# Optimization experiments

Measured on AMD Instinct MI355X. Metric: run time of the kernel, lower is better.

Reference implementation:

```python
import jax, jax.numpy as jnp
import numpy as np
import math

D_MODEL = 256
D_STATE = 16
D_CONV = 4
EXPAND = 2
N_HEADS = 4
D_INNER = EXPAND * D_MODEL          # 512
DT_RANK = (D_MODEL + 15) // 16      # 16
B_SZ, SEQ = 4, 2048


def setup_inputs() -> dict:
    key = jax.random.key(0)
    ks = jax.random.split(key, 12)
    rn = lambda i, shp, sc=0.02: jax.random.normal(ks[i], shp, dtype=jnp.float32) * sc
    x = jax.random.normal(ks[0], (B_SZ, SEQ, D_MODEL), dtype=jnp.float32)
    return dict(
        x=x,
        ln_g=jnp.ones((D_MODEL,), jnp.float32),
        ln_b=jnp.zeros((D_MODEL,), jnp.float32),
        W_in=rn(1, (D_MODEL, 2 * D_INNER)),
        conv_w=rn(2, (D_INNER, D_CONV), 0.1),
        conv_b=jnp.zeros((D_INNER,), jnp.float32),
        W_xproj=rn(3, (D_INNER, DT_RANK + 2 * D_STATE)),
        W_dt=rn(4, (DT_RANK, D_INNER), 0.1),
        b_dt=jnp.full((D_INNER,), -4.6, jnp.float32),  # softplus ~ 0.01 init
        A_log=jnp.log(jnp.tile(jnp.arange(1, D_STATE + 1, dtype=jnp.float32), (D_INNER, 1))),
        Dp=jnp.ones((D_INNER,), jnp.float32),
        W_out_m=rn(5, (D_INNER, D_MODEL)),
        W_qkv=rn(6, (D_MODEL, 3 * D_MODEL)),
        b_qkv=jnp.zeros((3 * D_MODEL,), jnp.float32),
        W_o=rn(7, (D_MODEL, D_MODEL)),
        b_o=jnp.zeros((D_MODEL,), jnp.float32),
        W_gate=rn(8, (2 * D_MODEL, D_MODEL)),
        b_gate=jnp.zeros((D_MODEL,), jnp.float32),
    )


def _sssd_forward(x, ln_g, ln_b, W_in, conv_w, conv_b, W_xproj, W_dt, b_dt,
                  A_log, Dp, W_out_m, W_qkv, b_qkv, W_o, b_o, W_gate, b_gate):
    B, L, D = x.shape
    # LayerNorm
    mu = x.mean(-1, keepdims=True)
    var = x.var(-1, keepdims=True)
    xn = (x - mu) * jax.lax.rsqrt(var + 1e-5) * ln_g + ln_b

    # ---- Mamba branch ----
    xz = xn @ W_in                      # (B,L,2*D_INNER)
    xm, z = jnp.split(xz, 2, axis=-1)
    # causal depthwise conv1d (kernel D_CONV)
    xp = jnp.pad(xm, ((0, 0), (D_CONV - 1, 0), (0, 0)))
    xc = conv_b + sum(xp[:, k:k + L, :] * conv_w[:, k] for k in range(D_CONV))
    xc = jax.nn.silu(xc)
    dbl = xc @ W_xproj                  # (B,L,DT_RANK+2*D_STATE)
    dt_in = dbl[..., :DT_RANK]
    Bm = dbl[..., DT_RANK:DT_RANK + D_STATE]
    Cm = dbl[..., DT_RANK + D_STATE:]
    dt = jax.nn.softplus(dt_in @ W_dt + b_dt)   # (B,L,D_INNER)
    A = -jnp.exp(A_log)                 # (D_INNER, D_STATE)

    def step(h, inp):
        x_t, dt_t, B_t, C_t = inp       # (B,Din),(B,Din),(B,N),(B,N)
        dA = jnp.exp(dt_t[..., None] * A)               # (B,Din,N)
        h = dA * h + (dt_t * x_t)[..., None] * B_t[:, None, :]
        y = jnp.einsum('bdn,bn->bd', h, C_t)
        return h, y

    h0 = jnp.zeros((B, D_INNER, D_STATE), x.dtype)
    xs = (jnp.swapaxes(xc, 0, 1), jnp.swapaxes(dt, 0, 1),
          jnp.swapaxes(Bm, 0, 1), jnp.swapaxes(Cm, 0, 1))
    _, ys = jax.lax.scan(step, h0, xs)
    y = jnp.swapaxes(ys, 0, 1) + xc * Dp
    y = y * jax.nn.silu(z)
    ssm_out = y @ W_out_m               # (B,L,D)

    # ---- MHSA branch (eval: no dropout) ----
    hd = D // N_HEADS
    qkv = xn @ W_qkv + b_qkv
    q, k, v = jnp.split(qkv, 3, axis=-1)
    sh = lambda t: t.reshape(B, L, N_HEADS, hd).transpose(0, 2, 1, 3)
    q, k, v = sh(q), sh(k), sh(v)
    scores = jnp.einsum('bhqd,bhkd->bhqk', q, k) * (1.0 / math.sqrt(hd))
    attn = jax.nn.softmax(scores, axis=-1)
    o = jnp.einsum('bhqk,bhkd->bhqd', attn, v).transpose(0, 2, 1, 3).reshape(B, L, D)
    attn_out = o @ W_o + b_o

    # ---- sigmoid gate fusion ----
    gate = jax.nn.sigmoid(jnp.concatenate([ssm_out, attn_out], axis=-1) @ W_gate + b_gate)
    fused = gate * ssm_out + (1.0 - gate) * attn_out
    return x + fused


def reference(x, ln_g, ln_b, W_in, conv_w, conv_b, W_xproj, W_dt, b_dt,
              A_log, Dp, W_out_m, W_qkv, b_qkv, W_o, b_o, W_gate, b_gate):
    return _sssd_forward(x, ln_g, ln_b, W_in, conv_w, conv_b, W_xproj, W_dt, b_dt,
                         A_log, Dp, W_out_m, W_qkv, b_qkv, W_o, b_o, W_gate, b_gate)
```

## Files before the change

kernel.cpp:

```cpp
#include <hip/hip_runtime.h>
#include <math.h>

#define B_SZ 4
#define SEQ 2048
#define DM 256
#define DI 512
#define DS 16
#define DTR 16
#define NH 4
#define HD 64
#define T_TOK (B_SZ*SEQ)
#define NCH 64
#define CL (SEQ/NCH)

typedef short bf16x8 __attribute__((ext_vector_type(8)));
typedef float f32x4  __attribute__((ext_vector_type(4)));
typedef unsigned short u16;

__device__ __forceinline__ float sigmoidf_(float x){ return 1.f/(1.f+__expf(-x)); }
__device__ __forceinline__ u16 f2bf(float x){
  unsigned int u = __float_as_uint(x);
  u += 0x7fffu + ((u>>16)&1u);
  return (u16)(u>>16);
}

__global__ __launch_bounds__(64) void tcvt_kernel(const float* __restrict__ src,
    u16* __restrict__ dst, int N, int K) {
  int n = blockIdx.x*64 + threadIdx.x;
  int k = blockIdx.y;
  dst[(size_t)n*K + k] = f2bf(src[(size_t)k*N + n]);
}

__global__ __launch_bounds__(64) void tcvt_pad_kernel(const float* __restrict__ src,
    u16* __restrict__ dst, int K, int Nvalid) {
  int n = threadIdx.x;
  int k = blockIdx.y;
  dst[(size_t)n*K + k] = (n < Nvalid) ? f2bf(src[(size_t)k*Nvalid + n]) : (u16)0;
}

__global__ __launch_bounds__(256) void ln_kernel(const float* __restrict__ x,
    const float* __restrict__ g, const float* __restrict__ b,
    u16* __restrict__ xn_bf) {
  int wid = threadIdx.x >> 6;
  int lane = threadIdx.x & 63;
  int token = blockIdx.x*4 + wid;
  const float* xr = x + (size_t)token*DM;
  float4 v = *(const float4*)&xr[lane*4];
  float s  = v.x+v.y+v.z+v.w;
  float ss = v.x*v.x+v.y*v.y+v.z*v.z+v.w*v.w;
  for (int m=1;m<64;m<<=1){ s += __shfl_xor(s,m); ss += __shfl_xor(ss,m); }
  float mu  = s * (1.f/DM);
  float var = ss*(1.f/DM) - mu*mu;
  float rs  = rsqrtf(var + 1e-5f);
  float4 gv = *(const float4*)&g[lane*4];
  float4 bv = *(const float4*)&b[lane*4];
  ushort4 o;
  o.x = f2bf((v.x-mu)*rs*gv.x + bv.x);
  o.y = f2bf((v.y-mu)*rs*gv.y + bv.y);
  o.z = f2bf((v.z-mu)*rs*gv.z + bv.z);
  o.w = f2bf((v.w-mu)*rs*gv.w + bv.w);
  *(ushort4*)&xn_bf[(size_t)token*DM + lane*4] = o;
}

template<int ACT>
__global__ __launch_bounds__(256) void gemm_mfma(const u16* __restrict__ A,
    const u16* __restrict__ Wt, const float* __restrict__ bias,
    float* __restrict__ C, u16* __restrict__ Cbf, int K, int ldc, int nvalid) {
  __shared__ u16 lds[12288];
  int tid = threadIdx.x;
  int m0 = blockIdx.y*128, n0 = blockIdx.x*64;
  int w = tid>>6, l = tid&63, lq = l&15, lg = l>>4;
  int wm = w>>1, wn = w&1;
  f32x4 acc[4][2] = {};
  for (int k0 = 0; k0 < K; k0 += 64) {
#pragma unroll
    for (int i=0;i<4;++i){
      int gid = i*256 + tid;
      int row = gid>>3, g = gid&7;
      *(bf16x8*)&lds[row*64 + ((g ^ (row&7))*8)] =
          *(const bf16x8*)&A[(size_t)(m0+row)*K + k0 + g*8];
    }
#pragma unroll
    for (int i=0;i<2;++i){
      int gid = i*256 + tid;
      int row = gid>>3, g = gid&7;
      *(bf16x8*)&lds[8192 + row*64 + ((g ^ (row&7))*8)] =
          *(const bf16x8*)&Wt[(size_t)(n0+row)*K + k0 + g*8];
    }
    __syncthreads();
#pragma unroll
    for (int ks=0;ks<2;++ks){
      bf16x8 af[4], bfv[2];
#pragma unroll
      for (int mi=0;mi<4;++mi){
        int row = wm*64 + mi*16 + lq;
        af[mi] = *(bf16x8*)&lds[row*64 + (((ks*4+lg) ^ (row&7))*8)];
      }
#pragma unroll
      for (int nj=0;nj<2;++nj){
        int row = wn*32 + nj*16 + lq;
        bfv[nj] = *(bf16x8*)&lds[8192 + row*64 + (((ks*4+lg) ^ (row&7))*8)];
      }
#pragma unroll
      for (int mi=0;mi<4;++mi)
#pragma unroll
        for (int nj=0;nj<2;++nj)
          acc[mi][nj] = __builtin_amdgcn_mfma_f32_16x16x32_bf16(af[mi], bfv[nj], acc[mi][nj], 0,0,0);
    }
    __syncthreads();
  }
#pragma unroll
  for (int mi=0;mi<4;++mi){
#pragma unroll
    for (int nj=0;nj<2;++nj){
#pragma unroll
      for (int r=0;r<4;++r){
        int row = m0 + wm*64 + mi*16 + lg*4 + r;
        int col = n0 + wn*32 + nj*16 + lq;
        if (col < nvalid) {
          float v = acc[mi][nj][r];
          if (bias) v += bias[col];
          if (ACT==1) v = sigmoidf_(v);
          if (C)   C[(size_t)row*ldc + col] = v;
          if (Cbf) Cbf[(size_t)row*ldc + col] = f2bf(v);
        }
      }
    }
  }
}

__global__ __launch_bounds__(256) void conv_kernel(const float* __restrict__ xz,
    const float* __restrict__ cw, const float* __restrict__ cb,
    float* __restrict__ xc, u16* __restrict__ xc_bf) {
  int idx = blockIdx.x*256 + threadIdx.x;
  int d = idx & (DI-1);
  int t = idx >> 9;
  int l = t & (SEQ-1);
  float acc = cb[d];
  float w0=cw[d*4+0], w1=cw[d*4+1], w2=cw[d*4+2], w3=cw[d*4+3];
  const float* base = xz + (size_t)t*1024 + d;
  if (l>=3) acc += base[-3*1024]*w0;
  if (l>=2) acc += base[-2*1024]*w1;
  if (l>=1) acc += base[-1*1024]*w2;
  acc += base[0]*w3;
  float v = acc * sigmoidf_(acc);
  xc[idx] = v;
  xc_bf[idx] = f2bf(v);
}

__global__ __launch_bounds__(256) void dt_kernel(const float* __restrict__ dbl,
    const float* __restrict__ Wdt, const float* __restrict__ bdt,
    float* __restrict__ dt) {
  __shared__ float sdbl[4][16];
  int wid = threadIdx.x>>6, lane = threadIdx.x&63;
  int token = blockIdx.x*4 + wid;
  if (lane < 16) sdbl[wid][lane] = dbl[(size_t)token*48 + lane];
  __syncthreads();
  float din[16];
#pragma unroll
  for (int k=0;k<16;++k) din[k] = sdbl[wid][k];
#pragma unroll
  for (int r=0;r<8;++r){
    int d = lane + r*64;
    float acc = bdt[d];
#pragma unroll
    for (int k=0;k<16;++k) acc += din[k]*Wdt[k*DI+d];
    float sp = (acc > 20.f) ? acc : log1pf(__expf(acc));
    dt[(size_t)token*DI+d] = sp;
  }
}

__global__ __launch_bounds__(512) void scan_p1(const float* __restrict__ xc,
    const float* __restrict__ dt, const float* __restrict__ dbl,
    const float* __restrict__ A_log, float* __restrict__ Pws, float* __restrict__ Hws) {
  __shared__ float sB[CL][16];
  int d = threadIdx.x;
  int bc = blockIdx.x;
  int b = bc >> 6, c = bc & 63;
  {
    int t = threadIdx.x >> 4, n = threadIdx.x & 15;
    sB[t][n] = dbl[((size_t)b*SEQ + c*CL + t)*48 + DTR + n];
  }
  __syncthreads();
  float An[16];
#pragma unroll
  for (int i=0;i<4;++i){
    float4 a = *(const float4*)&A_log[d*16 + i*4];
    An[i*4+0] = -__expf(a.x); An[i*4+1] = -__expf(a.y);
    An[i*4+2] = -__expf(a.z); An[i*4+3] = -__expf(a.w);
  }
  float h[16] = {};
  float P[16];
#pragma unroll
  for (int n=0;n<16;++n) P[n] = 1.f;
  size_t tok = (size_t)b*SEQ + c*CL;
  for (int t=0;t<CL;++t,++tok){
    float dtv = dt[tok*DI+d];
    float xcv = xc[tok*DI+d];
    float u = dtv*xcv;
    float4 B0 = *(float4*)&sB[t][0];
    float4 B1 = *(float4*)&sB[t][4];
    float4 B2 = *(float4*)&sB[t][8];
    float4 B3 = *(float4*)&sB[t][12];
    float Bv[16] = {B0.x,B0.y,B0.z,B0.w,B1.x,B1.y,B1.z,B1.w,
                    B2.x,B2.y,B2.z,B2.w,B3.x,B3.y,B3.z,B3.w};
#pragma unroll
    for (int n=0;n<16;++n){
      float e = __expf(dtv*An[n]);
      P[n] *= e;
      h[n] = e*h[n] + u*Bv[n];
    }
  }
  size_t base = (((size_t)b*NCH + c)*DI + d)*16;
#pragma unroll
  for (int n=0;n<16;++n){ Pws[base+n] = P[n]; Hws[base+n] = h[n]; }
}

__global__ __launch_bounds__(256) void scan_combine(const float* __restrict__ Pws,
    const float* __restrict__ Hws, float* __restrict__ H0ws) {
  int gid = blockIdx.x*256 + threadIdx.x;
  int b  = gid >> 13;
  int dn = gid & 8191;
  float h0 = 0.f;
#pragma unroll 4
  for (int c=0;c<NCH;++c){
    size_t idx = ((size_t)(b*NCH+c)<<13) + dn;
    H0ws[idx] = h0;
    h0 = Pws[idx]*h0 + Hws[idx];
  }
}

__global__ __launch_bounds__(512) void scan_p2(const float* __restrict__ xc,
    const float* __restrict__ dt, const float* __restrict__ dbl,
    const float* __restrict__ A_log, const float* __restrict__ Dp,
    const float* __restrict__ xz, const float* __restrict__ H0ws,
    u16* __restrict__ ygate_bf) {
  __shared__ float sBC[CL][32];
  int d = threadIdx.x;
  int bc = blockIdx.x;
  int b = bc >> 6, c = bc & 63;
#pragma unroll
  for (int i=0;i<2;++i){
    int idx = i*512 + threadIdx.x;
    int t = idx >> 5, q = idx & 31;
    sBC[t][q] = dbl[((size_t)b*SEQ + c*CL + t)*48 + DTR + q];
  }
  __syncthreads();
  float An[16];
#pragma unroll
  for (int i=0;i<4;++i){
    float4 a = *(const float4*)&A_log[d*16 + i*4];
    An[i*4+0] = -__expf(a.x); An[i*4+1] = -__expf(a.y);
    An[i*4+2] = -__expf(a.z); An[i*4+3] = -__expf(a.w);
  }
  float Dd = Dp[d];
  float h[16];
  size_t base = (((size_t)b*NCH + c)*DI + d)*16;
#pragma unroll
  for (int i=0;i<4;++i){
    float4 h4 = *(const float4*)&H0ws[base + i*4];
    h[i*4+0]=h4.x; h[i*4+1]=h4.y; h[i*4+2]=h4.z; h[i*4+3]=h4.w;
  }
  size_t tok = (size_t)b*SEQ + c*CL;
  for (int t=0;t<CL;++t,++tok){
    float dtv = dt[tok*DI+d];
    float xcv = xc[tok*DI+d];
    float zv  = xz[tok*1024 + DI + d];
    float u = dtv*xcv;
    float4 B0 = *(float4*)&sBC[t][0];
    float4 B1 = *(float4*)&sBC[t][4];
    float4 B2 = *(float4*)&sBC[t][8];
    float4 B3 = *(float4*)&sBC[t][12];
    float4 C0 = *(float4*)&sBC[t][16];
    float4 C1 = *(float4*)&sBC[t][20];
    float4 C2 = *(float4*)&sBC[t][24];
    float4 C3 = *(float4*)&sBC[t][28];
    float Bv[16] = {B0.x,B0.y,B0.z,B0.w,B1.x,B1.y,B1.z,B1.w,
                    B2.x,B2.y,B2.z,B2.w,B3.x,B3.y,B3.z,B3.w};
    float Cv[16] = {C0.x,C0.y,C0.z,C0.w,C1.x,C1.y,C1.z,C1.w,
                    C2.x,C2.y,C2.z,C2.w,C3.x,C3.y,C3.z,C3.w};
    float y = 0.f;
#pragma unroll
    for (int n=0;n<16;++n){
      float e = __expf(dtv*An[n]);
      h[n] = e*h[n] + u*Bv[n];
      y += h[n]*Cv[n];
    }
    y += xcv*Dd;
    ygate_bf[tok*DI + d] = f2bf(y * (zv*sigmoidf_(zv)));
  }
}

__global__ __launch_bounds__(256) void vt_kernel(const u16* __restrict__ qkvb,
    u16* __restrict__ vT) {
  int bh = blockIdx.y; int b = bh>>2, h = bh&3;
  int l0 = blockIdx.x*64;
  int d = threadIdx.x & 63;
  int oct = threadIdx.x >> 6;
  u16 tmp[16];
#pragma unroll
  for (int i=0;i<16;++i){
    int l = l0 + oct*16 + i;
    tmp[i] = qkvb[((size_t)b*SEQ + l)*768 + 512 + h*HD + d];
  }
  size_t dst = ((size_t)bh*HD + d)*SEQ + l0 + oct*16;
  *(bf16x8*)&vT[dst]   = *(bf16x8*)&tmp[0];
  *(bf16x8*)&vT[dst+8] = *(bf16x8*)&tmp[8];
}

__global__ __launch_bounds__(256) void attn_mfma_kernel(const u16* __restrict__ qkvb,
    const u16* __restrict__ vT,
    float* __restrict__ Opart, float* __restrict__ ml) {
  __shared__ u16 lds[12288];
  int bh = blockIdx.y; int b = bh>>2, h = bh&3;
  int s = blockIdx.z;
  int tid = threadIdx.x;
  int w = tid>>6, l = tid&63;
  int lq = l & 15;
  int lg = l >> 4;
  size_t bbase = (size_t)b*SEQ;
  size_t vbase = (size_t)bh*HD*SEQ;
  int q0 = blockIdx.x*64 + w*16;

  bf16x8 qf[2];
#pragma unroll
  for (int dsl=0; dsl<2; ++dsl)
    qf[dsl] = *(const bf16x8*)&qkvb[(bbase + q0 + lq)*768 + h*HD + lg*8 + dsl*32];

  float m_ = -1e30f, l_ = 0.f;
  f32x4 oacc[4] = {{0,0,0,0},{0,0,0,0},{0,0,0,0},{0,0,0,0}};
  int pbase = 8192 + w*1024;

  for (int kt=s*8; kt<s*8+8; ++kt){
    __syncthreads();
#pragma unroll
    for (int i=0;i<2;++i){
      int gid = i*256 + tid;
      int row = gid>>3, g = gid&7;
      *(bf16x8*)&lds[row*64 + ((g ^ (row&7))*8)] =
          *(const bf16x8*)&qkvb[(bbase + kt*64 + row)*768 + 256 + h*HD + g*8];
    }
#pragma unroll
    for (int i=0;i<2;++i){
      int gid = i*256 + tid;
      int row = gid>>3, g = gid&7;
      *(bf16x8*)&lds[4096 + row*64 + ((g ^ (row&7))*8)] =
          *(const bf16x8*)&vT[vbase + (size_t)row*SEQ + kt*64 + g*8];
    }
    __syncthreads();

    f32x4 sacc[4] = {{0,0,0,0},{0,0,0,0},{0,0,0,0},{0,0,0,0}};
    __builtin_amdgcn_s_setprio(1);
#pragma unroll
    for (int kg=0;kg<4;++kg){
#pragma unroll
      for (int dsl=0;dsl<2;++dsl){
        int row = kg*16 + lq;
        bf16x8 kf = *(bf16x8*)&lds[row*64 + (((dsl*4 + lg) ^ (row&7))*8)];
        sacc[kg] = __builtin_amdgcn_mfma_f32_16x16x32_bf16(kf, qf[dsl], sacc[kg], 0,0,0);
      }
    }
    __builtin_amdgcn_s_setprio(0);

    float tm = sacc[0][0];
#pragma unroll
    for (int kg=0;kg<4;++kg){
      float a = fmaxf(fmaxf(sacc[kg][0],sacc[kg][1]),fmaxf(sacc[kg][2],sacc[kg][3]));
      tm = fmaxf(tm, a);
    }
    tm *= 0.125f;
    tm = fmaxf(tm, __shfl_xor(tm,16));
    tm = fmaxf(tm, __shfl_xor(tm,32));
    float mn = fmaxf(m_, tm);
    float sc = __expf(m_ - mn);
    m_ = mn;
    float p[4][4];
    float ps = 0.f;
#pragma unroll
    for (int kg=0;kg<4;++kg)
#pragma unroll
      for (int r=0;r<4;++r){
        float pe = __expf(sacc[kg][r]*0.125f - mn);
        p[kg][r] = pe;
        ps += pe;
      }
    ps += __shfl_xor(ps,16);
    ps += __shfl_xor(ps,32);
    l_ = l_*sc + ps;
#pragma unroll
    for (int dg=0;dg<4;++dg){
      oacc[dg][0]*=sc; oacc[dg][1]*=sc; oacc[dg][2]*=sc; oacc[dg][3]*=sc;
    }

#pragma unroll
    for (int kg=0;kg<4;++kg)
#pragma unroll
      for (int rp=0;rp<2;++rp){
        unsigned pk = (unsigned)f2bf(p[kg][2*rp]) | ((unsigned)f2bf(p[kg][2*rp+1])<<16);
        int off = pbase + lq*64 + (((2*kg + (lg>>1)) ^ (lq&7))*8) + 4*(lg&1) + 2*rp;
        *(unsigned*)&lds[off] = pk;
      }

    __builtin_amdgcn_s_setprio(1);
#pragma unroll
    for (int ks=0;ks<2;++ks){
      bf16x8 pf = *(bf16x8*)&lds[pbase + lq*64 + (((ks*4 + lg) ^ (lq&7))*8)];
#pragma unroll
      for (int dg=0;dg<4;++dg){
        int row = dg*16 + lq;
        bf16x8 vf = *(bf16x8*)&lds[4096 + row*64 + (((ks*4 + lg) ^ (row&7))*8)];
        oacc[dg] = __builtin_amdgcn_mfma_f32_16x16x32_bf16(vf, pf, oacc[dg], 0,0,0);
      }
    }
    __builtin_amdgcn_s_setprio(0);
  }

  int sidx = bh*4 + s;
  size_t rb = ((size_t)sidx*SEQ + q0 + lq)*64;
#pragma unroll
  for (int dg=0;dg<4;++dg)
#pragma unroll
    for (int r=0;r<4;++r)
      Opart[rb + dg*16 + lg*4 + r] = oacc[dg][r];
  if (lg==0){
    ml[((size_t)sidx*SEQ + q0 + lq)*2    ] = m_;
    ml[((size_t)sidx*SEQ + q0 + lq)*2 + 1] = l_;
  }
}

__global__ __launch_bounds__(256) void attn_merge_kernel(const float* __restrict__ Opart,
    const float* __restrict__ ml, u16* __restrict__ attn_bf) {
  int w = threadIdx.x>>6, lane = threadIdx.x&63;
  int R = blockIdx.x*4 + w;
  int bh = R>>11, q = R&2047;
  float m[4], lv[4];
#pragma unroll
  for (int s=0;s<4;++s){
    m[s]  = ml[((size_t)(bh*4+s)*SEQ + q)*2];
    lv[s] = ml[((size_t)(bh*4+s)*SEQ + q)*2 + 1];
  }
  float ms = fmaxf(fmaxf(m[0],m[1]),fmaxf(m[2],m[3]));
  float o = 0.f, lsum = 0.f;
#pragma unroll
  for (int s=0;s<4;++s){
    float wsc = __expf(m[s]-ms);
    lsum += wsc*lv[s];
    o += wsc*Opart[((size_t)(bh*4+s)*SEQ + q)*64 + lane];
  }
  size_t token = (size_t)(bh>>2)*SEQ + q;
  attn_bf[token*DM + (bh&3)*HD + lane] = f2bf(o/lsum);
}

__global__ __launch_bounds__(256) void final_kernel(const float* __restrict__ x,
    const float* __restrict__ cat, const float* __restrict__ gate,
    float* __restrict__ out) {
  int idx = blockIdx.x*256 + threadIdx.x;
  int token = idx >> 6;
  int q = (idx & 63)*4;
  float4 g4 = *(const float4*)&gate[(size_t)token*DM + q];
  float4 s4 = *(const float4*)&cat[(size_t)token*512 + q];
  float4 a4 = *(const float4*)&cat[(size_t)token*512 + 256 + q];
  float4 x4 = *(const float4*)&x[(size_t)token*DM + q];
  float4 o;
  o.x = x4.x + g4.x*s4.x + (1.f-g4.x)*a4.x;
  o.y = x4.y + g4.y*s4.y + (1.f-g4.y)*a4.y;
  o.z = x4.z + g4.z*s4.z + (1.f-g4.z)*a4.z;
  o.w = x4.w + g4.w*s4.w + (1.f-g4.w)*a4.w;
  *(float4*)&out[(size_t)token*DM + q] = o;
}

extern "C" void kernel_launch(void* const* d_in, const int* in_sizes, int n_in,
                              void* d_out, int out_size, void* d_ws, size_t ws_size,
                              hipStream_t stream) {
  const float* x      = (const float*)d_in[0];
  const float* ln_g   = (const float*)d_in[1];
  const float* ln_b   = (const float*)d_in[2];
  const float* W_in   = (const float*)d_in[3];
  const float* conv_w = (const float*)d_in[4];
  const float* conv_b = (const float*)d_in[5];
  const float* W_xproj= (const float*)d_in[6];
  const float* W_dt   = (const float*)d_in[7];
  const float* b_dt   = (const float*)d_in[8];
  const float* A_log  = (const float*)d_in[9];
  const float* Dp     = (const float*)d_in[10];
  const float* W_out_m= (const float*)d_in[11];
  const float* W_qkv  = (const float*)d_in[12];
  const float* b_qkv  = (const float*)d_in[13];
  const float* W_o    = (const float*)d_in[14];
  const float* b_o    = (const float*)d_in[15];
  const float* W_gate = (const float*)d_in[16];
  const float* b_gate = (const float*)d_in[17];
  float* out = (float*)d_out;

  float* ws = (float*)d_ws;
  u16*   xn_bf   = (u16*)(ws);
  float* xz      = ws + 1048576;
  u16*   qkv_bf  = (u16*)(ws + 9437184);
  float* xc      = ws + 12582912;
  float* dblb    = ws + 16777216;
  float* dtb     = ws + 17170432;
  u16*   ygate_bf= (u16*)(ws + 21364736);
  u16*   attn_bf = (u16*)(ws + 23461888);
  float* catb    = ws + 24510464;
  u16*   catb_bf = (u16*)(ws + 28704768);
  float* gateb   = ws + 30801920;
  u16*   Wt_all  = (u16*)(ws + 32899072);
  float* Opart = xz;
  float* mlb   = (float*)xn_bf;
  u16*   vTb   = (u16*)dtb;
  u16*   xc_bf = ygate_bf;
  float* Pws   = catb;
  float* Hws   = catb + 2097152;
  float* H0ws  = catb + 4194304;

  u16* Wt_in   = Wt_all;
  u16* Wt_qkv  = Wt_all + 262144;
  u16* Wt_out  = Wt_all + 458752;
  u16* Wt_o    = Wt_all + 589824;
  u16* Wt_gate = Wt_all + 655360;
  u16* Wt_xp   = Wt_all + 786432;

  tcvt_kernel<<<dim3(16,256), 64, 0, stream>>>(W_in,    Wt_in,   1024, 256);
  tcvt_kernel<<<dim3(12,256), 64, 0, stream>>>(W_qkv,   Wt_qkv,   768, 256);
  tcvt_kernel<<<dim3(4,512),  64, 0, stream>>>(W_out_m, Wt_out,   256, 512);
  tcvt_kernel<<<dim3(4,256),  64, 0, stream>>>(W_o,     Wt_o,     256, 256);
  tcvt_kernel<<<dim3(4,512),  64, 0, stream>>>(W_gate,  Wt_gate,  256, 512);
  tcvt_pad_kernel<<<dim3(1,512), 64, 0, stream>>>(W_xproj, Wt_xp, 512, 48);

  ln_kernel<<<T_TOK/4, 256, 0, stream>>>(x, ln_g, ln_b, xn_bf);
  gemm_mfma<0><<<dim3(16,64), 256, 0, stream>>>(xn_bf, Wt_in, nullptr, xz, nullptr, 256, 1024, 1024);
  gemm_mfma<0><<<dim3(12,64), 256, 0, stream>>>(xn_bf, Wt_qkv, b_qkv, nullptr, qkv_bf, 256, 768, 768);
  conv_kernel<<<T_TOK*DI/256, 256, 0, stream>>>(xz, conv_w, conv_b, xc, xc_bf);
  gemm_mfma<0><<<dim3(1,64), 256, 0, stream>>>(xc_bf, Wt_xp, nullptr, dblb, nullptr, 512, 48, 48);
  dt_kernel<<<T_TOK/4, 256, 0, stream>>>(dblb, W_dt, b_dt, dtb);
  scan_p1<<<B_SZ*NCH, 512, 0, stream>>>(xc, dtb, dblb, A_log, Pws, Hws);
  scan_combine<<<128, 256, 0, stream>>>(Pws, Hws, H0ws);
  scan_p2<<<B_SZ*NCH, 512, 0, stream>>>(xc, dtb, dblb, A_log, Dp, xz, H0ws, ygate_bf);
  vt_kernel<<<dim3(SEQ/64, 16), 256, 0, stream>>>(qkv_bf, vTb);
  attn_mfma_kernel<<<dim3(SEQ/64, 16, 4), 256, 0, stream>>>(qkv_bf, vTb, Opart, mlb);
  attn_merge_kernel<<<8192, 256, 0, stream>>>(Opart, mlb, attn_bf);
  gemm_mfma<0><<<dim3(4,64), 256, 0, stream>>>(ygate_bf, Wt_out, nullptr, catb, catb_bf, 512, 512, 256);
  gemm_mfma<0><<<dim3(4,64), 256, 0, stream>>>(attn_bf, Wt_o, b_o, catb+256, catb_bf+256, 256, 512, 256);
  gemm_mfma<1><<<dim3(4,64), 256, 0, stream>>>(catb_bf, Wt_gate, b_gate, gateb, nullptr, 512, 256, 256);
  final_kernel<<<T_TOK*64/256, 256, 0, stream>>>(x, catb, gateb, out);
}
```

Before: 264.7 us.

## Store xz and conv output in bf16, fold softmax scale into Q, fuse final gating

The in-projection output and the conv output are now stored only in bf16, which halves the memory traffic through conv and both scan passes. The attention scale times log2(e) is folded into Q inside the QKV GEMM epilogue, so the kernel uses exp2 and rescales the running output only when the row max grows by more than 8. The final gating kernel is fused into the gate GEMM epilogue, and bf16 packing uses the v_cvt_pk_bf16_f32 instruction. Attention blocks are remapped to a swizzled grid order for cache locality. The cost is lower precision in the SSM inputs and the lazy-rescale approximation.

```diff
diff --git a/kernel.cpp b/kernel.cpp
--- a/kernel.cpp
+++ b/kernel.cpp
@@ -12,6 +12,7 @@
 #define T_TOK (B_SZ*SEQ)
 #define NCH 64
 #define CL (SEQ/NCH)
+#define QSCALE 0.18033688f
 
 typedef short bf16x8 __attribute__((ext_vector_type(8)));
 typedef float f32x4  __attribute__((ext_vector_type(4)));
@@ -22,6 +23,12 @@
   unsigned int u = __float_as_uint(x);
   u += 0x7fffu + ((u>>16)&1u);
   return (u16)(u>>16);
+}
+__device__ __forceinline__ float bf2f(u16 u){ return __uint_as_float(((unsigned)u)<<16); }
+__device__ __forceinline__ unsigned cvt_pk_bf16(float lo, float hi){
+  unsigned r;
+  asm("v_cvt_pk_bf16_f32 %0, %1, %2" : "=v"(r) : "v"(lo), "v"(hi));
+  return r;
 }
 
 __global__ __launch_bounds__(64) void tcvt_kernel(const float* __restrict__ src,
@@ -54,18 +61,18 @@
   float rs  = rsqrtf(var + 1e-5f);
   float4 gv = *(const float4*)&g[lane*4];
   float4 bv = *(const float4*)&b[lane*4];
-  ushort4 o;
-  o.x = f2bf((v.x-mu)*rs*gv.x + bv.x);
-  o.y = f2bf((v.y-mu)*rs*gv.y + bv.y);
-  o.z = f2bf((v.z-mu)*rs*gv.z + bv.z);
-  o.w = f2bf((v.w-mu)*rs*gv.w + bv.w);
-  *(ushort4*)&xn_bf[(size_t)token*DM + lane*4] = o;
+  uint2 o;
+  o.x = cvt_pk_bf16((v.x-mu)*rs*gv.x + bv.x, (v.y-mu)*rs*gv.y + bv.y);
+  o.y = cvt_pk_bf16((v.z-mu)*rs*gv.z + bv.z, (v.w-mu)*rs*gv.w + bv.w);
+  *(uint2*)&xn_bf[(size_t)token*DM + lane*4] = o;
 }
 
 template<int ACT>
 __global__ __launch_bounds__(256) void gemm_mfma(const u16* __restrict__ A,
     const u16* __restrict__ Wt, const float* __restrict__ bias,
-    float* __restrict__ C, u16* __restrict__ Cbf, int K, int ldc, int nvalid) {
+    float* __restrict__ C, u16* __restrict__ Cbf, int K, int ldc, int nvalid,
+    int qcols, float qscale, const float* __restrict__ xres,
+    const float* __restrict__ cat2) {
   __shared__ u16 lds[12288];
   int tid = threadIdx.x;
   int m0 = blockIdx.y*128, n0 = blockIdx.x*64;
@@ -120,32 +127,43 @@
         if (col < nvalid) {
           float v = acc[mi][nj][r];
           if (bias) v += bias[col];
-          if (ACT==1) v = sigmoidf_(v);
-          if (C)   C[(size_t)row*ldc + col] = v;
-          if (Cbf) Cbf[(size_t)row*ldc + col] = f2bf(v);
+          if (col < qcols) v *= qscale;
+          if (ACT==2) {
+            float g = sigmoidf_(v);
+            float sv = cat2[(size_t)row*512 + col];
+            float av = cat2[(size_t)row*512 + 256 + col];
+            C[(size_t)row*256 + col] = xres[(size_t)row*256 + col] + g*sv + (1.f-g)*av;
+          } else {
+            if (ACT==1) v = sigmoidf_(v);
+            if (C)   C[(size_t)row*ldc + col] = v;
+            if (Cbf) Cbf[(size_t)row*ldc + col] = f2bf(v);
+          }
         }
       }
     }
   }
 }
 
-__global__ __launch_bounds__(256) void conv_kernel(const float* __restrict__ xz,
+__global__ __launch_bounds__(256) void conv_kernel(const u16* __restrict__ xzb,
     const float* __restrict__ cw, const float* __restrict__ cb,
-    float* __restrict__ xc, u16* __restrict__ xc_bf) {
+    u16* __restrict__ xc_bf) {
   int idx = blockIdx.x*256 + threadIdx.x;
-  int d = idx & (DI-1);
-  int t = idx >> 9;
+  int d2 = (idx & 255)*2;
+  int t = idx >> 8;
   int l = t & (SEQ-1);
-  float acc = cb[d];
-  float w0=cw[d*4+0], w1=cw[d*4+1], w2=cw[d*4+2], w3=cw[d*4+3];
-  const float* base = xz + (size_t)t*1024 + d;
-  if (l>=3) acc += base[-3*1024]*w0;
-  if (l>=2) acc += base[-2*1024]*w1;
-  if (l>=1) acc += base[-1*1024]*w2;
-  acc += base[0]*w3;
-  float v = acc * sigmoidf_(acc);
-  xc[idx] = v;
-  xc_bf[idx] = f2bf(v);
+  float acc0 = cb[d2], acc1 = cb[d2+1];
+  float4 wA = *(const float4*)&cw[d2*4];
+  float4 wB = *(const float4*)&cw[d2*4+4];
+  const u16* base = xzb + (size_t)t*1024 + d2;
+  ushort2 v;
+  if (l>=3){ v = *(const ushort2*)&base[-3*1024]; acc0 += bf2f(v.x)*wA.x; acc1 += bf2f(v.y)*wB.x; }
+  if (l>=2){ v = *(const ushort2*)&base[-2*1024]; acc0 += bf2f(v.x)*wA.y; acc1 += bf2f(v.y)*wB.y; }
+  if (l>=1){ v = *(const ushort2*)&base[-1*1024]; acc0 += bf2f(v.x)*wA.z; acc1 += bf2f(v.y)*wB.z; }
+  v = *(const ushort2*)&base[0];
+  acc0 += bf2f(v.x)*wA.w; acc1 += bf2f(v.y)*wB.w;
+  float r0 = acc0 * sigmoidf_(acc0);
+  float r1 = acc1 * sigmoidf_(acc1);
+  *(unsigned*)&xc_bf[(size_t)t*DI + d2] = cvt_pk_bf16(r0, r1);
 }
 
 __global__ __launch_bounds__(256) void dt_kernel(const float* __restrict__ dbl,
@@ -170,7 +188,7 @@
   }
 }
 
-__global__ __launch_bounds__(512) void scan_p1(const float* __restrict__ xc,
+__global__ __launch_bounds__(512) void scan_p1(const u16* __restrict__ xc_bf,
     const float* __restrict__ dt, const float* __restrict__ dbl,
     const float* __restrict__ A_log, float* __restrict__ Pws, float* __restrict__ Hws) {
   __shared__ float sB[CL][16];
@@ -196,7 +214,7 @@
   size_t tok = (size_t)b*SEQ + c*CL;
   for (int t=0;t<CL;++t,++tok){
     float dtv = dt[tok*DI+d];
-    float xcv = xc[tok*DI+d];
+    float xcv = bf2f(xc_bf[tok*DI+d]);
     float u = dtv*xcv;
     float4 B0 = *(float4*)&sB[t][0];
     float4 B1 = *(float4*)&sB[t][4];
@@ -230,10 +248,10 @@
   }
 }
 
-__global__ __launch_bounds__(512) void scan_p2(const float* __restrict__ xc,
+__global__ __launch_bounds__(512) void scan_p2(const u16* __restrict__ xc_bf,
     const float* __restrict__ dt, const float* __restrict__ dbl,
     const float* __restrict__ A_log, const float* __restrict__ Dp,
-    const float* __restrict__ xz, const float* __restrict__ H0ws,
+    const u16* __restrict__ xzb, const float* __restrict__ H0ws,
     u16* __restrict__ ygate_bf) {
   __shared__ float sBC[CL][32];
   int d = threadIdx.x;
@@ -264,8 +282,8 @@
   size_t tok = (size_t)b*SEQ + c*CL;
   for (int t=0;t<CL;++t,++tok){
     float dtv = dt[tok*DI+d];
-    float xcv = xc[tok*DI+d];
-    float zv  = xz[tok*1024 + DI + d];
+    float xcv = bf2f(xc_bf[tok*DI+d]);
+    float zv  = bf2f(xzb[tok*1024 + DI + d]);
     float u = dtv*xcv;
     float4 B0 = *(float4*)&sBC[t][0];
     float4 B1 = *(float4*)&sBC[t][4];
@@ -312,15 +330,19 @@
     const u16* __restrict__ vT,
     float* __restrict__ Opart, float* __restrict__ ml) {
   __shared__ u16 lds[12288];
-  int bh = blockIdx.y; int b = bh>>2, h = bh&3;
-  int s = blockIdx.z;
+  int H = blockIdx.x + 32*blockIdx.y + 512*(int)blockIdx.z;
+  int cx = H & 7, k = H >> 3;
+  int xq = k & 31;
+  int G  = cx*8 + (k >> 5);
+  int bh = G & 15, s = G >> 4;
+  int b = bh>>2, h = bh&3;
   int tid = threadIdx.x;
   int w = tid>>6, l = tid&63;
   int lq = l & 15;
   int lg = l >> 4;
   size_t bbase = (size_t)b*SEQ;
   size_t vbase = (size_t)bh*HD*SEQ;
-  int q0 = blockIdx.x*64 + w*16;
+  int q0 = xq*64 + w*16;
 
   bf16x8 qf[2];
 #pragma unroll
@@ -368,35 +390,37 @@
       float a = fmaxf(fmaxf(sacc[kg][0],sacc[kg][1]),fmaxf(sacc[kg][2],sacc[kg][3]));
       tm = fmaxf(tm, a);
     }
-    tm *= 0.125f;
     tm = fmaxf(tm, __shfl_xor(tm,16));
     tm = fmaxf(tm, __shfl_xor(tm,32));
-    float mn = fmaxf(m_, tm);
-    float sc = __expf(m_ - mn);
-    m_ = mn;
+    if (__any(tm - m_ > 8.f)) {
+      float mn = fmaxf(m_, tm);
+      float sc = exp2f(m_ - mn);
+      m_ = mn;
+      l_ *= sc;
+#pragma unroll
+      for (int dg=0;dg<4;++dg){
+        oacc[dg][0]*=sc; oacc[dg][1]*=sc; oacc[dg][2]*=sc; oacc[dg][3]*=sc;
+      }
+    }
     float p[4][4];
     float ps = 0.f;
 #pragma unroll
     for (int kg=0;kg<4;++kg)
 #pragma unroll
       for (int r=0;r<4;++r){
-        float pe = __expf(sacc[kg][r]*0.125f - mn);
+        float pe = exp2f(sacc[kg][r] - m_);
         p[kg][r] = pe;
         ps += pe;
       }
     ps += __shfl_xor(ps,16);
     ps += __shfl_xor(ps,32);
-    l_ = l_*sc + ps;
-#pragma unroll
-    for (int dg=0;dg<4;++dg){
-      oacc[dg][0]*=sc; oacc[dg][1]*=sc; oacc[dg][2]*=sc; oacc[dg][3]*=sc;
-    }
+    l_ += ps;
 
 #pragma unroll
     for (int kg=0;kg<4;++kg)
 #pragma unroll
       for (int rp=0;rp<2;++rp){
-        unsigned pk = (unsigned)f2bf(p[kg][2*rp]) | ((unsigned)f2bf(p[kg][2*rp+1])<<16);
+        unsigned pk = cvt_pk_bf16(p[kg][2*rp], p[kg][2*rp+1]);
         int off = pbase + lq*64 + (((2*kg + (lg>>1)) ^ (lq&7))*8) + 4*(lg&1) + 2*rp;
         *(unsigned*)&lds[off] = pk;
       }
@@ -443,30 +467,12 @@
   float o = 0.f, lsum = 0.f;
 #pragma unroll
   for (int s=0;s<4;++s){
-    float wsc = __expf(m[s]-ms);
+    float wsc = exp2f(m[s]-ms);
     lsum += wsc*lv[s];
     o += wsc*Opart[((size_t)(bh*4+s)*SEQ + q)*64 + lane];
   }
   size_t token = (size_t)(bh>>2)*SEQ + q;
   attn_bf[token*DM + (bh&3)*HD + lane] = f2bf(o/lsum);
-}
-
-__global__ __launch_bounds__(256) void final_kernel(const float* __restrict__ x,
-    const float* __restrict__ cat, const float* __restrict__ gate,
-    float* __restrict__ out) {
-  int idx = blockIdx.x*256 + threadIdx.x;
-  int token = idx >> 6;
-  int q = (idx & 63)*4;
-  float4 g4 = *(const float4*)&gate[(size_t)token*DM + q];
-  float4 s4 = *(const float4*)&cat[(size_t)token*512 + q];
-  float4 a4 = *(const float4*)&cat[(size_t)token*512 + 256 + q];
-  float4 x4 = *(const float4*)&x[(size_t)token*DM + q];
-  float4 o;
-  o.x = x4.x + g4.x*s4.x + (1.f-g4.x)*a4.x;
-  o.y = x4.y + g4.y*s4.y + (1.f-g4.y)*a4.y;
-  o.z = x4.z + g4.z*s4.z + (1.f-g4.z)*a4.z;
-  o.w = x4.w + g4.w*s4.w + (1.f-g4.w)*a4.w;
-  *(float4*)&out[(size_t)token*DM + q] = o;
 }
 
 extern "C" void kernel_launch(void* const* d_in, const int* in_sizes, int n_in,
@@ -494,9 +500,9 @@
 
   float* ws = (float*)d_ws;
   u16*   xn_bf   = (u16*)(ws);
-  float* xz      = ws + 1048576;
+  u16*   xzb     = (u16*)(ws + 1048576);
   u16*   qkv_bf  = (u16*)(ws + 9437184);
-  float* xc      = ws + 12582912;
+  u16*   xc_bf   = (u16*)(ws + 12582912);
   float* dblb    = ws + 16777216;
   float* dtb     = ws + 17170432;
   u16*   ygate_bf= (u16*)(ws + 21364736);
@@ -505,13 +511,13 @@
   u16*   catb_bf = (u16*)(ws + 28704768);
   float* gateb   = ws + 30801920;
   u16*   Wt_all  = (u16*)(ws + 32899072);
-  float* Opart = xz;
+  float* Opart = ws + 1048576;
   float* mlb   = (float*)xn_bf;
   u16*   vTb   = (u16*)dtb;
-  u16*   xc_bf = ygate_bf;
   float* Pws   = catb;
   float* Hws   = catb + 2097152;
   float* H0ws  = catb + 4194304;
+  (void)gateb;
 
   u16* Wt_in   = Wt_all;
   u16* Wt_qkv  = Wt_all + 262144;
@@ -528,19 +534,18 @@
   tcvt_pad_kernel<<<dim3(1,512), 64, 0, stream>>>(W_xproj, Wt_xp, 512, 48);
 
   ln_kernel<<<T_TOK/4, 256, 0, stream>>>(x, ln_g, ln_b, xn_bf);
-  gemm_mfma<0><<<dim3(16,64), 256, 0, stream>>>(xn_bf, Wt_in, nullptr, xz, nullptr, 256, 1024, 1024);
-  gemm_mfma<0><<<dim3(12,64), 256, 0, stream>>>(xn_bf, Wt_qkv, b_qkv, nullptr, qkv_bf, 256, 768, 768);
-  conv_kernel<<<T_TOK*DI/256, 256, 0, stream>>>(xz, conv_w, conv_b, xc, xc_bf);
-  gemm_mfma<0><<<dim3(1,64), 256, 0, stream>>>(xc_bf, Wt_xp, nullptr, dblb, nullptr, 512, 48, 48);
+  gemm_mfma<0><<<dim3(16,64), 256, 0, stream>>>(xn_bf, Wt_in, nullptr, nullptr, xzb, 256, 1024, 1024, 0, 1.f, nullptr, nullptr);
+  gemm_mfma<0><<<dim3(12,64), 256, 0, stream>>>(xn_bf, Wt_qkv, b_qkv, nullptr, qkv_bf, 256, 768, 768, 256, QSCALE, nullptr, nullptr);
+  conv_kernel<<<T_TOK, 256, 0, stream>>>(xzb, conv_w, conv_b, xc_bf);
+  gemm_mfma<0><<<dim3(1,64), 256, 0, stream>>>(xc_bf, Wt_xp, nullptr, dblb, nullptr, 512, 48, 48, 0, 1.f, nullptr, nullptr);
   dt_kernel<<<T_TOK/4, 256, 0, stream>>>(dblb, W_dt, b_dt, dtb);
-  scan_p1<<<B_SZ*NCH, 512, 0, stream>>>(xc, dtb, dblb, A_log, Pws, Hws);
+  scan_p1<<<B_SZ*NCH, 512, 0, stream>>>(xc_bf, dtb, dblb, A_log, Pws, Hws);
   scan_combine<<<128, 256, 0, stream>>>(Pws, Hws, H0ws);
-  scan_p2<<<B_SZ*NCH, 512, 0, stream>>>(xc, dtb, dblb, A_log, Dp, xz, H0ws, ygate_bf);
+  scan_p2<<<B_SZ*NCH, 512, 0, stream>>>(xc_bf, dtb, dblb, A_log, Dp, xzb, H0ws, ygate_bf);
   vt_kernel<<<dim3(SEQ/64, 16), 256, 0, stream>>>(qkv_bf, vTb);
   attn_mfma_kernel<<<dim3(SEQ/64, 16, 4), 256, 0, stream>>>(qkv_bf, vTb, Opart, mlb);
   attn_merge_kernel<<<8192, 256, 0, stream>>>(Opart, mlb, attn_bf);
-  gemm_mfma<0><<<dim3(4,64), 256, 0, stream>>>(ygate_bf, Wt_out, nullptr, catb, catb_bf, 512, 512, 256);
-  gemm_mfma<0><<<dim3(4,64), 256, 0, stream>>>(attn_bf, Wt_o, b_o, catb+256, catb_bf+256, 256, 512, 256);
-  gemm_mfma<1><<<dim3(4,64), 256, 0, stream>>>(catb_bf, Wt_gate, b_gate, gateb, nullptr, 512, 256, 256);
-  final_kernel<<<T_TOK*64/256, 256, 0, stream>>>(x, catb, gateb, out);
-}
+  gemm_mfma<0><<<dim3(4,64), 256, 0, stream>>>(ygate_bf, Wt_out, nullptr, catb, catb_bf, 512, 512, 256, 0, 1.f, nullptr, nullptr);
+  gemm_mfma<0><<<dim3(4,64), 256, 0, stream>>>(attn_bf, Wt_o, b_o, catb+256, catb_bf+256, 256, 512, 256, 0, 1.f, nullptr, nullptr);
+  gemm_mfma<2><<<dim3(4,64), 256, 0, stream>>>(catb_bf, Wt_gate, b_gate, out, nullptr, 512, 256, 256, 0, 1.f, x, catb);
+}
```

Result: no change. 260.3 us (-1.6%).
